# Kernel optimization log

Hardware: AMD Instinct MI355X
Metric: run time of the kernel (lower is better)

The kernel has to match this reference:

```python
import jax, jax.numpy as jnp
import numpy as np


def setup_inputs() -> dict:
    key = jax.random.key(0)
    k1, k2 = jax.random.split(key)
    B, C, H, W = 32, 64, 64, 64
    K = 512
    z_e = jax.random.normal(k1, (B, C, H, W), dtype=jnp.float32)
    # codebook initialized uniform(-1/K, 1/K) as in the torch module
    codebook = jax.random.uniform(k2, (K, C), dtype=jnp.float32,
                                  minval=-1.0 / K, maxval=1.0 / K)
    return {"z_e": z_e, "codebook": codebook}


def reference(z_e, codebook):
    B, C, H, W = z_e.shape
    commitment_cost = 0.25
    # [B*H*W, C]
    z_flat = jnp.transpose(z_e, (0, 2, 3, 1)).reshape(-1, C)
    dists = (jnp.sum(z_flat * z_flat, axis=1, keepdims=True)
             + jnp.sum(codebook * codebook, axis=1)
             - 2.0 * jnp.matmul(z_flat, codebook.T))
    encoding_indices = jnp.argmin(dists, axis=1)  # [N] int
    z_q = codebook[encoding_indices].reshape(B, H, W, C)
    z_q = jnp.transpose(z_q, (0, 3, 1, 2))  # [B, C, H, W]
    q_loss = jnp.mean((z_q - jax.lax.stop_gradient(z_e)) ** 2)
    e_loss = jnp.mean((z_e - jax.lax.stop_gradient(z_q)) ** 2)
    loss = q_loss + commitment_cost * e_loss
    # straight-through estimator
    z_q_st = z_e + jax.lax.stop_gradient(z_q - z_e)
    return (z_q_st, encoding_indices, loss)
```

## Files before the change

### kernel.cpp

```cpp
#include <hip/hip_runtime.h>
#include <cfloat>

typedef __attribute__((ext_vector_type(8))) short short8;
typedef __attribute__((ext_vector_type(4))) float f32x4;

constexpr int C_DIM    = 64;
constexpr int K_CODES  = 512;
constexpr int HW       = 4096;
constexpr int CHW      = 262144;
constexpr int NPTS     = 131072;
constexpr int ZQ_SIZE  = 8388608;
constexpr int IDX_OFF  = ZQ_SIZE;
constexpr int LOSS_OFF = ZQ_SIZE + NPTS;
constexpr int TILE     = 128;
constexpr int CHUNK    = 128;
constexpr int NSLOT    = 16;
constexpr size_t WS_BF16 = (size_t)K_CODES * C_DIM * 2;
constexpr size_t WS_NEED = WS_BF16 + (size_t)K_CODES * 4;

__device__ __forceinline__ unsigned short f32_to_bf16_rne(float f) {
    unsigned u = __float_as_uint(f);
    unsigned r = u + 0x7fffu + ((u >> 16) & 1u);
    return (unsigned short)(r >> 16);
}

template <int STRIDE>
__device__ __forceinline__ float np_sumsq64(const float* __restrict__ a) {
    float r[8];
#pragma unroll
    for (int j = 0; j < 8; ++j) { const float v = a[j * STRIDE]; r[j] = __fmul_rn(v, v); }
#pragma unroll
    for (int i = 8; i < 64; i += 8)
#pragma unroll
        for (int j = 0; j < 8; ++j) {
            const float v = a[(i + j) * STRIDE];
            r[j] = __fadd_rn(r[j], __fmul_rn(v, v));
        }
    return __fadd_rn(
        __fadd_rn(__fadd_rn(r[0], r[1]), __fadd_rn(r[2], r[3])),
        __fadd_rn(__fadd_rn(r[4], r[5]), __fadd_rn(r[6], r[7])));
}

__global__ void vq_zero(float* __restrict__ out) { out[LOSS_OFF] = 0.0f; }

__global__ void vq_prep(const float* __restrict__ cb, unsigned short* __restrict__ wsb,
                        float* __restrict__ wsB, float* __restrict__ out) {
    const int gid = blockIdx.x * 256 + threadIdx.x;
    wsb[gid] = f32_to_bf16_rne(cb[gid]);
    if (gid < K_CODES) wsB[gid] = np_sumsq64<1>(cb + gid * C_DIM);
    if (gid == 0) out[LOSS_OFF] = 0.0f;
}

__global__ __launch_bounds__(256, 4) void vq_idx(const float* __restrict__ ze,
                                                 const float* __restrict__ cb,
                                                 float* __restrict__ out,
                                                 const unsigned short* __restrict__ wsb,
                                                 const float* __restrict__ wsB,
                                                 int use_ws)
{
    __shared__ unsigned short eh[CHUNK * C_DIM];
    __shared__ float  BsL[K_CODES];
    __shared__ float  As[TILE];
    __shared__ unsigned short cand[TILE * NSLOT];
    __shared__ int    cnt[TILE];
    __shared__ int    bestk[TILE];
    __shared__ double lred[4];

    const int tid  = threadIdx.x;
    const int lane = tid & 63, w = tid >> 6;
    const int quad = lane >> 4, l15 = lane & 15;
    const int n0   = blockIdx.x * TILE;
    const int b    = n0 >> 12, hw0 = n0 & (HW - 1);
    const float* zebase = ze + b * CHW + hw0;

    if (use_ws) { for (int k = tid; k < K_CODES; k += 256) BsL[k] = wsB[k]; }
    else        { for (int k = tid; k < K_CODES; k += 256) BsL[k] = np_sumsq64<1>(cb + k * C_DIM); }
    if (tid < TILE) { As[tid] = np_sumsq64<HW>(zebase + tid); cnt[tid] = 0; }
    __syncthreads();

    short8 afr[2][2];
    float  A_pt[2][4], thr[2][4], runmin[2][4];
#pragma unroll
    for (int rt = 0; rt < 2; ++rt) {
        const int pt = w * 32 + rt * 16 + l15;
#pragma unroll
        for (int kc = 0; kc < 2; ++kc) {
            union { unsigned short s[8]; short8 v; } u;
#pragma unroll
            for (int j = 0; j < 8; ++j) {
                const int c = kc * 32 + quad * 8 + j;
                u.s[j] = f32_to_bf16_rne(zebase[c * HW + pt]);
            }
            afr[rt][kc] = u.v;
        }
#pragma unroll
        for (int r = 0; r < 4; ++r) {
            A_pt[rt][r]   = As[w * 32 + rt * 16 + quad * 4 + r];
            runmin[rt][r] = FLT_MAX;
        }
    }

    auto stage = [&](int ch) {
        const int row = tid >> 1, half = tid & 1;
        uint4* base = (uint4*)eh;
        if (use_ws) {
            const uint4* src = (const uint4*)(wsb + (size_t)(ch * CHUNK + row) * C_DIM);
#pragma unroll
            for (int i = 0; i < 4; ++i) {
                const int sl = half * 4 + i;
                base[row * 8 + (sl ^ (row & 7))] = src[sl];
            }
        } else {
            const float4* src = (const float4*)(cb + (size_t)(ch * CHUNK + row) * C_DIM);
#pragma unroll
            for (int i = 0; i < 4; ++i) {
                const int sl = half * 4 + i;
                const float4 f0 = src[2 * sl], f1 = src[2 * sl + 1];
                uint4 o;
                o.x = (unsigned)f32_to_bf16_rne(f0.x) | ((unsigned)f32_to_bf16_rne(f0.y) << 16);
                o.y = (unsigned)f32_to_bf16_rne(f0.z) | ((unsigned)f32_to_bf16_rne(f0.w) << 16);
                o.z = (unsigned)f32_to_bf16_rne(f1.x) | ((unsigned)f32_to_bf16_rne(f1.y) << 16);
                o.w = (unsigned)f32_to_bf16_rne(f1.z) | ((unsigned)f32_to_bf16_rne(f1.w) << 16);
                base[row * 8 + (sl ^ (row & 7))] = o;
            }
        }
    };

    for (int ch = 0; ch < 4; ++ch) {
        __syncthreads(); stage(ch); __syncthreads();
        const uint4* ebase = (const uint4*)eh;
        for (int tile = 0; tile < 8; ++tile) {
            const int cl = tile * 16 + l15;
            const short8 b0 = *(const short8*)&ebase[cl * 8 + ((quad    ) ^ (cl & 7))];
            const short8 b1 = *(const short8*)&ebase[cl * 8 + ((quad + 4) ^ (cl & 7))];
            const float bs = BsL[ch * CHUNK + cl];
#pragma unroll
            for (int rt = 0; rt < 2; ++rt) {
                f32x4 acc = {0.f, 0.f, 0.f, 0.f};
                acc = __builtin_amdgcn_mfma_f32_16x16x32_bf16(afr[rt][0], b0, acc, 0, 0, 0);
                acc = __builtin_amdgcn_mfma_f32_16x16x32_bf16(afr[rt][1], b1, acc, 0, 0, 0);
#pragma unroll
                for (int r = 0; r < 4; ++r) {
                    const float D = fmaf(-2.f, acc[r], __fadd_rn(A_pt[rt][r], bs));
                    runmin[rt][r] = fminf(runmin[rt][r], D);
                }
            }
        }
    }
#pragma unroll
    for (int rt = 0; rt < 2; ++rt)
#pragma unroll
        for (int r = 0; r < 4; ++r) {
            float v = runmin[rt][r];
#pragma unroll
            for (int m = 1; m < 16; m <<= 1) v = fminf(v, __shfl_xor(v, m, 64));
            thr[rt][r] = v + (4e-4f * sqrtf(A_pt[rt][r]) + 3e-4f);
        }

    for (int ch = 0; ch < 4; ++ch) {
        __syncthreads(); stage(ch); __syncthreads();
        const uint4* ebase = (const uint4*)eh;
        for (int tile = 0; tile < 8; ++tile) {
            const int cl = tile * 16 + l15;
            const short8 b0 = *(const short8*)&ebase[cl * 8 + ((quad    ) ^ (cl & 7))];
            const short8 b1 = *(const short8*)&ebase[cl * 8 + ((quad + 4) ^ (cl & 7))];
            const float bs = BsL[ch * CHUNK + cl];
#pragma unroll
            for (int rt = 0; rt < 2; ++rt) {
                f32x4 acc = {0.f, 0.f, 0.f, 0.f};
                acc = __builtin_amdgcn_mfma_f32_16x16x32_bf16(afr[rt][0], b0, acc, 0, 0, 0);
                acc = __builtin_amdgcn_mfma_f32_16x16x32_bf16(afr[rt][1], b1, acc, 0, 0, 0);
#pragma unroll
                for (int r = 0; r < 4; ++r) {
                    const float D = fmaf(-2.f, acc[r], __fadd_rn(A_pt[rt][r], bs));
                    if (D <= thr[rt][r]) {
                        const int pt = w * 32 + rt * 16 + quad * 4 + r;
                        const int p = atomicAdd(&cnt[pt], 1);
                        if (p < NSLOT) cand[pt * NSLOT + p] = (unsigned short)(ch * CHUNK + cl);
                    }
                }
            }
        }
    }
    __syncthreads();

    if (tid < TILE) {
        const float Av = As[tid];
        const int c = cnt[tid];
        float bD = FLT_MAX; int bK = K_CODES;
        if (c <= NSLOT) {
            for (int i = 0; i < c; ++i) {
                const int k = cand[tid * NSLOT + i];
                const float* er = cb + k * C_DIM;
                float M = 0.f;
#pragma unroll
                for (int cc = 0; cc < 64; ++cc) M = fmaf(zebase[cc * HW + tid], er[cc], M);
                const float D = fmaf(-2.f, M, __fadd_rn(Av, BsL[k]));
                if (D < bD || (D == bD && k < bK)) { bD = D; bK = k; }
            }
        } else {
            for (int k = 0; k < K_CODES; ++k) {
                const float* er = cb + k * C_DIM;
                float M = 0.f;
#pragma unroll
                for (int cc = 0; cc < 64; ++cc) M = fmaf(zebase[cc * HW + tid], er[cc], M);
                const float D = fmaf(-2.f, M, __fadd_rn(Av, BsL[k]));
                if (D < bD) { bD = D; bK = k; }
            }
        }
        bestk[tid] = bK;
        out[IDX_OFF + n0 + tid] = (float)bK;
    }
    __syncthreads();

    double ls = 0.0;
#pragma unroll
    for (int it = 0; it < 8; ++it) {
        const int task = tid + 256 * it;
        const int c = task >> 5, q = task & 31;
        const float4 xz = *(const float4*)(zebase + c * HW + 4 * q);
        float o[4];
#pragma unroll
        for (int j = 0; j < 4; ++j) {
            const int k = bestk[4 * q + j];
            const float ev = cb[k * C_DIM + c];
            const float xv = (j == 0) ? xz.x : (j == 1) ? xz.y : (j == 2) ? xz.z : xz.w;
            const float d = __fsub_rn(ev, xv);
            o[j] = __fadd_rn(xv, d);
            ls = fma((double)d, (double)d, ls);
        }
        *(float4*)(out + b * CHW + c * HW + hw0 + 4 * q) = make_float4(o[0], o[1], o[2], o[3]);
    }
#pragma unroll
    for (int off = 32; off > 0; off >>= 1) ls += __shfl_xor(ls, off, 64);
    if ((tid & 63) == 0) lred[w] = ls;
    __syncthreads();
    if (tid == 0)
        atomicAdd(out + LOSS_OFF,
                  (float)((lred[0] + lred[1] + lred[2] + lred[3]) * (1.25 / (double)ZQ_SIZE)));
}

extern "C" void kernel_launch(void* const* d_in, const int* in_sizes, int n_in,
                              void* d_out, int out_size, void* d_ws, size_t ws_size,
                              hipStream_t stream) {
    (void)in_sizes; (void)n_in; (void)out_size;
    const float* ze = (const float*)d_in[0];
    const float* cb = (const float*)d_in[1];
    float* out = (float*)d_out;
    const int use_ws = (ws_size >= WS_NEED) ? 1 : 0;
    unsigned short* wsb = (unsigned short*)d_ws;
    float* wsB = (float*)((char*)d_ws + WS_BF16);

    if (use_ws) vq_prep<<<(K_CODES * C_DIM) / 256, 256, 0, stream>>>(cb, wsb, wsB, out);
    else        vq_zero<<<1, 1, 0, stream>>>(out);
    vq_idx<<<NPTS / TILE, 256, 0, stream>>>(ze, cb, out, wsb, wsB, use_ws);
}
```

Before: 140.6 us.

## Halve point tile, parallelize refinement across lanes, cache z tile in LDS

Shrinks the per-block point tile from 128 to 64 so there are twice as many blocks, with one 16-row MFMA tile per wave. Splits the per-point norm computation and the exact fp32 candidate refinement across four lanes per point, and handles the full-scan fallback with a whole wave. Copies the z tile into LDS, reusing the codebook staging buffer, so refinement and output no longer reread global memory. Reorders the passes so the last staged codebook chunk is reused at the start of the second pass, saving one stage. The cost is more blocks that each reload the codebook and norms, plus extra synchronisation.

```diff
diff --git a/kernel.cpp b/kernel.cpp
--- a/kernel.cpp
+++ b/kernel.cpp
@@ -12,7 +12,7 @@
 constexpr int ZQ_SIZE  = 8388608;
 constexpr int IDX_OFF  = ZQ_SIZE;
 constexpr int LOSS_OFF = ZQ_SIZE + NPTS;
-constexpr int TILE     = 128;
+constexpr int TILE     = 64;
 constexpr int CHUNK    = 128;
 constexpr int NSLOT    = 16;
 constexpr size_t WS_BF16 = (size_t)K_CODES * C_DIM * 2;
@@ -39,6 +39,19 @@
     return __fadd_rn(
         __fadd_rn(__fadd_rn(r[0], r[1]), __fadd_rn(r[2], r[3])),
         __fadd_rn(__fadd_rn(r[4], r[5]), __fadd_rn(r[6], r[7])));
+}
+
+__device__ __forceinline__ float np_sumsq64_quarter_hw(const float* __restrict__ a, int jj) {
+    const int j0 = 2 * jj, j1 = 2 * jj + 1;
+    float rA = __fmul_rn(a[j0 * HW], a[j0 * HW]);
+    float rB = __fmul_rn(a[j1 * HW], a[j1 * HW]);
+#pragma unroll
+    for (int i = 8; i < 64; i += 8) {
+        const float vA = a[(i + j0) * HW], vB = a[(i + j1) * HW];
+        rA = __fadd_rn(rA, __fmul_rn(vA, vA));
+        rB = __fadd_rn(rB, __fmul_rn(vB, vB));
+    }
+    return __fadd_rn(rA, rB);
 }
 
 __global__ void vq_zero(float* __restrict__ out) { out[LOSS_OFF] = 0.0f; }
@@ -58,7 +71,7 @@
                                                  const float* __restrict__ wsB,
                                                  int use_ws)
 {
-    __shared__ unsigned short eh[CHUNK * C_DIM];
+    __shared__ __align__(16) unsigned short eh[CHUNK * C_DIM];
     __shared__ float  BsL[K_CODES];
     __shared__ float  As[TILE];
     __shared__ unsigned short cand[TILE * NSLOT];
@@ -72,33 +85,6 @@
     const int n0   = blockIdx.x * TILE;
     const int b    = n0 >> 12, hw0 = n0 & (HW - 1);
     const float* zebase = ze + b * CHW + hw0;
-
-    if (use_ws) { for (int k = tid; k < K_CODES; k += 256) BsL[k] = wsB[k]; }
-    else        { for (int k = tid; k < K_CODES; k += 256) BsL[k] = np_sumsq64<1>(cb + k * C_DIM); }
-    if (tid < TILE) { As[tid] = np_sumsq64<HW>(zebase + tid); cnt[tid] = 0; }
-    __syncthreads();
-
-    short8 afr[2][2];
-    float  A_pt[2][4], thr[2][4], runmin[2][4];
-#pragma unroll
-    for (int rt = 0; rt < 2; ++rt) {
-        const int pt = w * 32 + rt * 16 + l15;
-#pragma unroll
-        for (int kc = 0; kc < 2; ++kc) {
-            union { unsigned short s[8]; short8 v; } u;
-#pragma unroll
-            for (int j = 0; j < 8; ++j) {
-                const int c = kc * 32 + quad * 8 + j;
-                u.s[j] = f32_to_bf16_rne(zebase[c * HW + pt]);
-            }
-            afr[rt][kc] = u.v;
-        }
-#pragma unroll
-        for (int r = 0; r < 4; ++r) {
-            A_pt[rt][r]   = As[w * 32 + rt * 16 + quad * 4 + r];
-            runmin[rt][r] = FLT_MAX;
-        }
-    }
 
     auto stage = [&](int ch) {
         const int row = tid >> 1, half = tid & 1;
@@ -126,99 +112,158 @@
         }
     };
 
+    if (use_ws) { for (int k = tid; k < K_CODES; k += 256) BsL[k] = wsB[k]; }
+    else        { for (int k = tid; k < K_CODES; k += 256) BsL[k] = np_sumsq64<1>(cb + k * C_DIM); }
+    if (tid < TILE) cnt[tid] = 0;
+    stage(0);
+
+    short8 afr[2];
+    float  A_pt[4], thr[4], runmin[4];
+#pragma unroll
+    for (int kc = 0; kc < 2; ++kc) {
+        union { unsigned short s[8]; short8 v; } u;
+#pragma unroll
+        for (int j = 0; j < 8; ++j) {
+            const int c = kc * 32 + quad * 8 + j;
+            u.s[j] = f32_to_bf16_rne(zebase[c * HW + w * 16 + l15]);
+        }
+        afr[kc] = u.v;
+    }
+#pragma unroll
+    for (int r = 0; r < 4; ++r) runmin[r] = FLT_MAX;
+
+    {
+        const int ptA = tid >> 2, jj = tid & 3;
+        const float q = np_sumsq64_quarter_hw(zebase + ptA, jj);
+        const float q01 = __fadd_rn(q, __shfl_xor(q, 1, 64));
+        const float tot = __fadd_rn(q01, __shfl_xor(q01, 2, 64));
+        if (jj == 0) As[ptA] = tot;
+    }
+    __syncthreads();
+#pragma unroll
+    for (int r = 0; r < 4; ++r) A_pt[r] = As[w * 16 + quad * 4 + r];
+
     for (int ch = 0; ch < 4; ++ch) {
-        __syncthreads(); stage(ch); __syncthreads();
+        if (ch) { __syncthreads(); stage(ch); __syncthreads(); }
         const uint4* ebase = (const uint4*)eh;
+#pragma unroll 4
         for (int tile = 0; tile < 8; ++tile) {
             const int cl = tile * 16 + l15;
             const short8 b0 = *(const short8*)&ebase[cl * 8 + ((quad    ) ^ (cl & 7))];
             const short8 b1 = *(const short8*)&ebase[cl * 8 + ((quad + 4) ^ (cl & 7))];
             const float bs = BsL[ch * CHUNK + cl];
-#pragma unroll
-            for (int rt = 0; rt < 2; ++rt) {
-                f32x4 acc = {0.f, 0.f, 0.f, 0.f};
-                acc = __builtin_amdgcn_mfma_f32_16x16x32_bf16(afr[rt][0], b0, acc, 0, 0, 0);
-                acc = __builtin_amdgcn_mfma_f32_16x16x32_bf16(afr[rt][1], b1, acc, 0, 0, 0);
-#pragma unroll
-                for (int r = 0; r < 4; ++r) {
-                    const float D = fmaf(-2.f, acc[r], __fadd_rn(A_pt[rt][r], bs));
-                    runmin[rt][r] = fminf(runmin[rt][r], D);
-                }
-            }
-        }
-    }
-#pragma unroll
-    for (int rt = 0; rt < 2; ++rt)
-#pragma unroll
-        for (int r = 0; r < 4; ++r) {
-            float v = runmin[rt][r];
-#pragma unroll
-            for (int m = 1; m < 16; m <<= 1) v = fminf(v, __shfl_xor(v, m, 64));
-            thr[rt][r] = v + (4e-4f * sqrtf(A_pt[rt][r]) + 3e-4f);
-        }
-
-    for (int ch = 0; ch < 4; ++ch) {
-        __syncthreads(); stage(ch); __syncthreads();
+            f32x4 acc = {0.f, 0.f, 0.f, 0.f};
+            acc = __builtin_amdgcn_mfma_f32_16x16x32_bf16(afr[0], b0, acc, 0, 0, 0);
+            acc = __builtin_amdgcn_mfma_f32_16x16x32_bf16(afr[1], b1, acc, 0, 0, 0);
+#pragma unroll
+            for (int r = 0; r < 4; ++r) {
+                const float D = fmaf(-2.f, acc[r], __fadd_rn(A_pt[r], bs));
+                runmin[r] = fminf(runmin[r], D);
+            }
+        }
+    }
+#pragma unroll
+    for (int r = 0; r < 4; ++r) {
+        float v = runmin[r];
+#pragma unroll
+        for (int m = 1; m < 16; m <<= 1) v = fminf(v, __shfl_xor(v, m, 64));
+        thr[r] = v + (4e-4f * sqrtf(A_pt[r]) + 3e-4f);
+    }
+
+    auto scan_push = [&](int ch) {
         const uint4* ebase = (const uint4*)eh;
+#pragma unroll 4
         for (int tile = 0; tile < 8; ++tile) {
             const int cl = tile * 16 + l15;
             const short8 b0 = *(const short8*)&ebase[cl * 8 + ((quad    ) ^ (cl & 7))];
             const short8 b1 = *(const short8*)&ebase[cl * 8 + ((quad + 4) ^ (cl & 7))];
             const float bs = BsL[ch * CHUNK + cl];
-#pragma unroll
-            for (int rt = 0; rt < 2; ++rt) {
-                f32x4 acc = {0.f, 0.f, 0.f, 0.f};
-                acc = __builtin_amdgcn_mfma_f32_16x16x32_bf16(afr[rt][0], b0, acc, 0, 0, 0);
-                acc = __builtin_amdgcn_mfma_f32_16x16x32_bf16(afr[rt][1], b1, acc, 0, 0, 0);
-#pragma unroll
-                for (int r = 0; r < 4; ++r) {
-                    const float D = fmaf(-2.f, acc[r], __fadd_rn(A_pt[rt][r], bs));
-                    if (D <= thr[rt][r]) {
-                        const int pt = w * 32 + rt * 16 + quad * 4 + r;
-                        const int p = atomicAdd(&cnt[pt], 1);
-                        if (p < NSLOT) cand[pt * NSLOT + p] = (unsigned short)(ch * CHUNK + cl);
-                    }
+            f32x4 acc = {0.f, 0.f, 0.f, 0.f};
+            acc = __builtin_amdgcn_mfma_f32_16x16x32_bf16(afr[0], b0, acc, 0, 0, 0);
+            acc = __builtin_amdgcn_mfma_f32_16x16x32_bf16(afr[1], b1, acc, 0, 0, 0);
+#pragma unroll
+            for (int r = 0; r < 4; ++r) {
+                const float D = fmaf(-2.f, acc[r], __fadd_rn(A_pt[r], bs));
+                if (D <= thr[r]) {
+                    const int pt = w * 16 + quad * 4 + r;
+                    const int p = atomicAdd(&cnt[pt], 1);
+                    if (p < NSLOT) cand[pt * NSLOT + p] = (unsigned short)(ch * CHUNK + cl);
                 }
             }
         }
-    }
-    __syncthreads();
-
-    if (tid < TILE) {
-        const float Av = As[tid];
-        const int c = cnt[tid];
-        float bD = FLT_MAX; int bK = K_CODES;
+    };
+    scan_push(3);
+    for (int ch = 0; ch < 3; ++ch) {
+        __syncthreads(); stage(ch); __syncthreads();
+        scan_push(ch);
+    }
+    __syncthreads();
+
+    float* zef = (float*)eh;
+#pragma unroll
+    for (int it = 0; it < 4; ++it) {
+        const int task = tid + 256 * it;
+        const int c = task >> 4, q = task & 15;
+        const float4 v = *(const float4*)(zebase + c * HW + 4 * q);
+        *(float4*)&zef[c * TILE + 4 * q] = v;
+    }
+    __syncthreads();
+
+    {
+        const int pt = tid >> 2, sub = tid & 3;
+        const int c = cnt[pt];
         if (c <= NSLOT) {
-            for (int i = 0; i < c; ++i) {
-                const int k = cand[tid * NSLOT + i];
+            const float Av = As[pt];
+            float bD = FLT_MAX; int bK = K_CODES;
+            for (int i = sub; i < c; i += 4) {
+                const int k = cand[pt * NSLOT + i];
                 const float* er = cb + k * C_DIM;
                 float M = 0.f;
 #pragma unroll
-                for (int cc = 0; cc < 64; ++cc) M = fmaf(zebase[cc * HW + tid], er[cc], M);
+                for (int cc = 0; cc < 64; ++cc) M = fmaf(zef[cc * TILE + pt], er[cc], M);
                 const float D = fmaf(-2.f, M, __fadd_rn(Av, BsL[k]));
                 if (D < bD || (D == bD && k < bK)) { bD = D; bK = k; }
             }
-        } else {
-            for (int k = 0; k < K_CODES; ++k) {
-                const float* er = cb + k * C_DIM;
-                float M = 0.f;
-#pragma unroll
-                for (int cc = 0; cc < 64; ++cc) M = fmaf(zebase[cc * HW + tid], er[cc], M);
-                const float D = fmaf(-2.f, M, __fadd_rn(Av, BsL[k]));
-                if (D < bD) { bD = D; bK = k; }
-            }
-        }
-        bestk[tid] = bK;
-        out[IDX_OFF + n0 + tid] = (float)bK;
+#pragma unroll
+            for (int off = 1; off < 4; off <<= 1) {
+                const float oD = __shfl_xor(bD, off, 64);
+                const int   oK = __shfl_xor(bK, off, 64);
+                if (oD < bD || (oD == bD && oK < bK)) { bD = oD; bK = oK; }
+            }
+            if (sub == 0) { bestk[pt] = bK; out[IDX_OFF + n0 + pt] = (float)bK; }
+        }
+    }
+    __syncthreads();
+
+    for (int pp = 0; pp < 16; ++pp) {
+        const int pt = w * 16 + pp;
+        if (cnt[pt] <= NSLOT) continue;
+        const float Av = As[pt];
+        float bD = FLT_MAX; int bK = K_CODES;
+        for (int k = lane; k < K_CODES; k += 64) {
+            const float* er = cb + k * C_DIM;
+            float M = 0.f;
+#pragma unroll
+            for (int cc = 0; cc < 64; ++cc) M = fmaf(zef[cc * TILE + pt], er[cc], M);
+            const float D = fmaf(-2.f, M, __fadd_rn(Av, BsL[k]));
+            if (D < bD || (D == bD && k < bK)) { bD = D; bK = k; }
+        }
+#pragma unroll
+        for (int off = 1; off < 64; off <<= 1) {
+            const float oD = __shfl_xor(bD, off, 64);
+            const int   oK = __shfl_xor(bK, off, 64);
+            if (oD < bD || (oD == bD && oK < bK)) { bD = oD; bK = oK; }
+        }
+        if (lane == 0) { bestk[pt] = bK; out[IDX_OFF + n0 + pt] = (float)bK; }
     }
     __syncthreads();
 
     double ls = 0.0;
 #pragma unroll
-    for (int it = 0; it < 8; ++it) {
+    for (int it = 0; it < 4; ++it) {
         const int task = tid + 256 * it;
-        const int c = task >> 5, q = task & 31;
-        const float4 xz = *(const float4*)(zebase + c * HW + 4 * q);
+        const int c = task >> 4, q = task & 15;
+        const float4 xz = *(const float4*)&zef[c * TILE + 4 * q];
         float o[4];
 #pragma unroll
         for (int j = 0; j < 4; ++j) {
```

New measurement: 145.8 us. +3.8%, slower.
